# Kernel tuning notes

Measured on AMD Instinct MI355X. Metric: run time of the kernel, lower is better.

The kernel has to match this reference:

```python
import math
import jax, jax.numpy as jnp
import numpy as np

EPS = 1e-5

def _ln(x, g, b, axes):
    # LayerNormalization4D / 4DCF: mean/var (unbiased=False) over `axes`
    mu = x.mean(axis=axes, keepdims=True)
    var = ((x - mu) ** 2).mean(axis=axes, keepdims=True)
    return (x - mu) / jnp.sqrt(var + EPS) * g + b

def _prelu(x, a):
    return jnp.where(x >= 0, x, a * x)

def _unfold(x, ks, hs):
    # x: [N, C, Q] -> [N, L, C*ks]; patch layout (c, k) matches F.unfold
    N, C, Qd = x.shape
    L = (Qd - ks) // hs + 1
    idx = jnp.arange(L) * hs
    p = x[:, :, idx[:, None] + jnp.arange(ks)]  # [N, C, L, ks]
    return p.transpose(0, 2, 1, 3).reshape(N, L, C * ks)

def _lstm_dir(xs, Wi, Wh, bi, bh, H):
    # xs: [N, L, Cin]; torch gate order i, f, g, o
    xg = jnp.einsum('nlc,gc->nlg', xs, Wi) + bi + bh  # [N, L, 4H]
    def step(carry, gt):
        h, c = carry
        g = gt + h @ Wh.T
        i, f, gg, o = jnp.split(g, 4, axis=-1)
        c = jax.nn.sigmoid(f) * c + jax.nn.sigmoid(i) * jnp.tanh(gg)
        h = jax.nn.sigmoid(o) * jnp.tanh(c)
        return (h, c), h
    N = xs.shape[0]
    z = jnp.zeros((N, H), xs.dtype)
    _, hs = jax.lax.scan(step, (z, z), jnp.swapaxes(xg, 0, 1))
    return jnp.swapaxes(hs, 0, 1)

def _bilstm(x, wih, whh, bih, bhh):
    H = whh.shape[-1]
    f = _lstm_dir(x, wih[0], whh[0], bih[0], bhh[0], H)
    bk = _lstm_dir(x[:, ::-1], wih[1], whh[1], bih[1], bhh[1], H)[:, ::-1]
    return jnp.concatenate([f, bk], axis=-1)

def _convT1d(x, w, b):
    # x: [N, I, L]; w: [I, O, K] (torch ConvTranspose1d layout); stride 1
    K = w.shape[2]
    w2 = jnp.transpose(w, (1, 0, 2))[:, :, ::-1]
    y = jax.lax.conv_general_dilated(x, w2, (1,), [(K - 1, K - 1)],
                                     dimension_numbers=('NCH', 'OIH', 'NCH'))
    return y + b[None, :, None]

def _forward(x, mouth, intra_g, intra_b, intra_wih, intra_whh, intra_bih, intra_bhh,
             intra_lw, intra_lb, inter_g, inter_b, inter_wih, inter_whh, inter_bih,
             inter_bhh, inter_lw, inter_lb, qw, qb, qa, qg, qbe, kw, kb, ka, kg, kbe,
             vw, vb, va, vg, vbe, pw, pb, pa, pg, pbe):
    emb_ks, emb_hs = 4, 1
    B, C, oT, oQ = x.shape
    T = math.ceil((oT - emb_ks) / emb_hs) * emb_hs + emb_ks
    Qd = math.ceil((oQ - emb_ks) / emb_hs) * emb_hs + emb_ks
    x = jnp.pad(x, ((0, 0), (0, 0), (0, T - oT), (0, Qd - oQ)))
    inp = x
    # ---- intra (biLSTM along freq axis) ----
    h = _ln(inp, intra_g[None, :, None, None], intra_b[None, :, None, None], (1,))
    h = h.transpose(0, 2, 1, 3).reshape(B * T, C, Qd)
    h = _unfold(h, emb_ks, emb_hs)                          # [B*T, L, C*ks]
    h = _bilstm(h, intra_wih, intra_whh, intra_bih, intra_bhh)
    h = _convT1d(h.transpose(0, 2, 1), intra_lw, intra_lb)  # [B*T, C, Qd]
    intra = h.reshape(B, T, C, Qd).transpose(0, 2, 1, 3) + inp
    # ---- inter (biLSTM along time axis) ----
    h = _ln(intra, inter_g[None, :, None, None], inter_b[None, :, None, None], (1,))
    h = h.transpose(0, 3, 1, 2).reshape(B * Qd, C, T)
    h = _unfold(h, emb_ks, emb_hs)
    h = _bilstm(h, inter_wih, inter_whh, inter_bih, inter_bhh)
    h = _convT1d(h.transpose(0, 2, 1), inter_lw, inter_lb)  # [B*Qd, C, T]
    inter = h.reshape(B, Qd, C, T).transpose(0, 2, 3, 1) + intra
    inter = inter[..., :oT, :oQ]                             # [B, C, oT, oQ]
    # ---- multi-head full self-attention over time (conv1x1 QKV per head) ----
    NH = qw.shape[0]
    def qkv(w, b_, a_, g_, be_):
        y = jnp.einsum('bctf,hec->hbetf', inter, w) + b_[:, None, :, None, None]
        y = _prelu(y, a_[:, None, None, None, None])
        return _ln(y, g_[:, None, :, None, :], be_[:, None, :, None, :], (2, 4))
    Qh = qkv(qw, qb, qa, qg, qbe)   # [H, B, E, T, F]
    Kh = qkv(kw, kb, ka, kg, kbe)
    Vh = qkv(vw, vb, va, vg, vbe)   # [H, B, D, T, F]
    E = Qh.shape[2]; D = Vh.shape[2]; F = oQ
    q2 = Qh.transpose(0, 1, 3, 2, 4).reshape(NH, B, oT, E * F)
    k2 = Kh.transpose(0, 1, 3, 2, 4).reshape(NH, B, oT, E * F)
    v2 = Vh.transpose(0, 1, 3, 2, 4).reshape(NH, B, oT, D * F)
    scale = 1.0 / jnp.sqrt(jnp.asarray(E * F, x.dtype))
    attn = jax.nn.softmax(jnp.einsum('hbte,hbse->hbts', q2, k2) * scale, axis=-1)
    o = jnp.einsum('hbts,hbsd->hbtd', attn, v2).reshape(NH, B, oT, D, F)
    o = o.transpose(1, 0, 3, 2, 4).reshape(B, NH * D, oT, F)
    # ---- concat projection ----
    p = jnp.einsum('bctf,oc->botf', o, pw) + pb[None, :, None, None]
    p = _prelu(p, pa)
    p = _ln(p, pg[None, :, None, :], pbe[None, :, None, :], (1, 3))
    return p + inter

def setup_inputs() -> dict:
    key = jax.random.key(0)
    keys = iter(jax.random.split(key, 48))
    f32 = jnp.float32
    def nrm(shape, s=0.05):
        return jax.random.normal(next(keys), shape, f32) * s
    B, C, T, F = 2, 48, 512, 65
    K, H, NH, E = 4, 192, 4, 8
    Cin = C * K
    D = C // NH
    return {
        'x': jax.random.normal(next(keys), (B, C, T, F), f32),
        'mouth': jax.random.normal(next(keys), (B, 64), f32),
        'intra_g': jnp.ones((C,), f32), 'intra_b': jnp.zeros((C,), f32),
        'intra_wih': nrm((2, 4 * H, Cin)), 'intra_whh': nrm((2, 4 * H, H)),
        'intra_bih': nrm((2, 4 * H)), 'intra_bhh': nrm((2, 4 * H)),
        'intra_lw': nrm((2 * H, C, K)), 'intra_lb': nrm((C,)),
        'inter_g': jnp.ones((C,), f32), 'inter_b': jnp.zeros((C,), f32),
        'inter_wih': nrm((2, 4 * H, Cin)), 'inter_whh': nrm((2, 4 * H, H)),
        'inter_bih': nrm((2, 4 * H)), 'inter_bhh': nrm((2, 4 * H)),
        'inter_lw': nrm((2 * H, C, K)), 'inter_lb': nrm((C,)),
        'qw': nrm((NH, E, C)), 'qb': nrm((NH, E)), 'qa': 0.25 * jnp.ones((NH,), f32),
        'qg': jnp.ones((NH, E, F), f32), 'qbe': jnp.zeros((NH, E, F), f32),
        'kw': nrm((NH, E, C)), 'kb': nrm((NH, E)), 'ka': 0.25 * jnp.ones((NH,), f32),
        'kg': jnp.ones((NH, E, F), f32), 'kbe': jnp.zeros((NH, E, F), f32),
        'vw': nrm((NH, D, C)), 'vb': nrm((NH, D)), 'va': 0.25 * jnp.ones((NH,), f32),
        'vg': jnp.ones((NH, D, F), f32), 'vbe': jnp.zeros((NH, D, F), f32),
        'pw': nrm((C, C)), 'pb': nrm((C,)), 'pa': jnp.float32(0.25),
        'pg': jnp.ones((C, F), f32), 'pbe': jnp.zeros((C, F), f32),
    }

def reference(x, mouth, intra_g, intra_b, intra_wih, intra_whh, intra_bih, intra_bhh,
              intra_lw, intra_lb, inter_g, inter_b, inter_wih, inter_whh, inter_bih,
              inter_bhh, inter_lw, inter_lb, qw, qb, qa, qg, qbe, kw, kb, ka, kg, kbe,
              vw, vb, va, vg, vbe, pw, pb, pa, pg, pbe):
    return _forward(x, mouth, intra_g, intra_b, intra_wih, intra_whh, intra_bih,
                    intra_bhh, intra_lw, intra_lb, inter_g, inter_b, inter_wih,
                    inter_whh, inter_bih, inter_bhh, inter_lw, inter_lb, qw, qb, qa,
                    qg, qbe, kw, kb, ka, kg, kbe, vw, vb, va, vg, vbe, pw, pb, pa,
                    pg, pbe)
```

## Files before the change

### kernel.cpp

```cpp
#include <hip/hip_runtime.h>
#include <hip/hip_bf16.h>

typedef __bf16 bf16x8 __attribute__((ext_vector_type(8)));
typedef unsigned short u16x8 __attribute__((ext_vector_type(8)));
typedef float f32x4 __attribute__((ext_vector_type(4)));

#define DEV static __device__ __forceinline__

DEV unsigned short f2bf(float f){
  __hip_bfloat16 h = __float2bfloat16(f);
  return __builtin_bit_cast(unsigned short, h);
}
DEV float b2f(unsigned short u){
  return __bfloat162float(__builtin_bit_cast(__hip_bfloat16, u));
}
DEV float sig2(float xs){
  return __builtin_amdgcn_rcpf(1.0f + __builtin_amdgcn_exp2f(-xs));
}
DEV float tanh2s(float xs){
  return 1.0f - 2.0f*__builtin_amdgcn_rcpf(__builtin_amdgcn_exp2f(xs + xs) + 1.0f);
}
DEV float tanh_n(float x){
  return 1.0f - 2.0f*__builtin_amdgcn_rcpf(__builtin_amdgcn_exp2f(x * 2.885390082f) + 1.0f);
}
DEV void lds_barrier(){
  asm volatile("s_waitcnt lgkmcnt(0)\ns_barrier" ::: "memory");
}


__global__ void zero16(uint4* p, size_t n){
  size_t i = (size_t)blockIdx.x*blockDim.x + threadIdx.x;
  size_t st = (size_t)gridDim.x*blockDim.x;
  uint4 z = make_uint4(0u,0u,0u,0u);
  for (; i < n; i += st) p[i] = z;
}

__global__ void cast_bf(const float* __restrict__ s, unsigned short* __restrict__ d, int n, float scale){
  int i = blockIdx.x*256 + threadIdx.x;
  if (i < n) d[i] = f2bf(s[i]*scale);
}

__global__ void cast_wi(const float* __restrict__ s, unsigned short* __restrict__ d, float scale){
  int i = blockIdx.x*256 + threadIdx.x;
  if (i < 294912){
    int dn = i/192, k = i - dn*192;
    int c = k >> 2, kk = k & 3;
    d[(size_t)dn*192 + kk*48 + c] = f2bf(s[i]*scale);
  }
}

__global__ void bias_comb(const float* __restrict__ a, const float* __restrict__ b,
                          float* __restrict__ d, int n, float scale){
  int i = blockIdx.x*256 + threadIdx.x;
  if (i < n) d[i] = (a[i] + b[i])*scale;
}

__global__ void lwt_build(const float* __restrict__ lw, unsigned short* __restrict__ lwt){
  int i = blockIdx.x*256 + threadIdx.x;
  if (i < 384*48*4){
    int m = i / 192; int rest = i - m*192; int c = rest >> 2; int k = rest & 3;
    lwt[(size_t)c*1536 + k*384 + m] = f2bf(lw[i]);
  }
}

__global__ __launch_bounds__(256) void ln_unf_intra(
    const float* __restrict__ in, const float* __restrict__ g,
    const float* __restrict__ be, unsigned short* __restrict__ unf)
{
  int bt = blockIdx.x; int b = bt >> 9, t = bt & 511;
  __shared__ float v[48][66];
  __shared__ float mu[65], rs[65];
  __shared__ float g_l[48], b_l[48];
  const float* base = in + (size_t)b*(48*512*65) + (size_t)t*65;
  for (int i = threadIdx.x; i < 48*65; i += 256){
    int c = i/65, q = i - c*65;
    v[c][q] = base[(size_t)c*(512*65) + q];
  }
  if (threadIdx.x < 48){ g_l[threadIdx.x] = g[threadIdx.x]; b_l[threadIdx.x] = be[threadIdx.x]; }
  __syncthreads();
  if (threadIdx.x < 65){
    int q = threadIdx.x; float s=0.f, s2=0.f;
    #pragma unroll
    for (int c = 0; c < 48; c++){ float x = v[c][q]; s += x; s2 += x*x; }
    float m = s*(1.0f/48.0f);
    mu[q] = m; rs[q] = rsqrtf(s2*(1.0f/48.0f) - m*m + 1e-5f);
  }
  __syncthreads();
  unsigned short* orow = unf + (size_t)(b*512 + t)*62*192;
  for (int idx = threadIdx.x; idx < 62*24; idx += 256){
    int l = idx/24, jg = idx - l*24;
    int kk = jg/6, c0 = (jg - kk*6)*8;
    int q = l + kk;
    ushort4 p0, p1;
    float mq = mu[q], rq = rs[q];
    p0.x = f2bf((v[c0+0][q]-mq)*rq*g_l[c0+0] + b_l[c0+0]);
    p0.y = f2bf((v[c0+1][q]-mq)*rq*g_l[c0+1] + b_l[c0+1]);
    p0.z = f2bf((v[c0+2][q]-mq)*rq*g_l[c0+2] + b_l[c0+2]);
    p0.w = f2bf((v[c0+3][q]-mq)*rq*g_l[c0+3] + b_l[c0+3]);
    p1.x = f2bf((v[c0+4][q]-mq)*rq*g_l[c0+4] + b_l[c0+4]);
    p1.y = f2bf((v[c0+5][q]-mq)*rq*g_l[c0+5] + b_l[c0+5]);
    p1.z = f2bf((v[c0+6][q]-mq)*rq*g_l[c0+6] + b_l[c0+6]);
    p1.w = f2bf((v[c0+7][q]-mq)*rq*g_l[c0+7] + b_l[c0+7]);
    *(ushort4*)(orow + (size_t)l*192 + kk*48 + c0) = p0;
    *(ushort4*)(orow + (size_t)l*192 + kk*48 + c0 + 4) = p1;
  }
}

__global__ __launch_bounds__(256) void ln_unf_inter(
    const float* __restrict__ in, const float* __restrict__ g,
    const float* __restrict__ be, unsigned short* __restrict__ unf)
{
  int bt = blockIdx.x; int b = bt >> 9, t = bt & 511;
  __shared__ float v[48][66];
  __shared__ float mu[65], rs[65];
  __shared__ float g_l[48], b_l[48];
  const float* base = in + (size_t)b*(48*512*65) + (size_t)t*65;
  for (int i = threadIdx.x; i < 48*65; i += 256){
    int c = i/65, q = i - c*65;
    v[c][q] = base[(size_t)c*(512*65) + q];
  }
  if (threadIdx.x < 48){ g_l[threadIdx.x] = g[threadIdx.x]; b_l[threadIdx.x] = be[threadIdx.x]; }
  __syncthreads();
  if (threadIdx.x < 65){
    int q = threadIdx.x; float s=0.f, s2=0.f;
    #pragma unroll
    for (int c = 0; c < 48; c++){ float x = v[c][q]; s += x; s2 += x*x; }
    float m = s*(1.0f/48.0f);
    mu[q] = m; rs[q] = rsqrtf(s2*(1.0f/48.0f) - m*m + 1e-5f);
  }
  __syncthreads();
  for (int idx = threadIdx.x; idx < 4*65*6; idx += 256){
    int s = idx/390;
    int rem = idx - s*390;
    int q = rem/6, c0 = (rem - q*6)*8;
    int l = t - 3 + s, kk = 3 - s;
    if (l < 0 || l > 508) continue;
    float mq = mu[q], rq = rs[q];
    ushort4 p0, p1;
    p0.x = f2bf((v[c0+0][q]-mq)*rq*g_l[c0+0] + b_l[c0+0]);
    p0.y = f2bf((v[c0+1][q]-mq)*rq*g_l[c0+1] + b_l[c0+1]);
    p0.z = f2bf((v[c0+2][q]-mq)*rq*g_l[c0+2] + b_l[c0+2]);
    p0.w = f2bf((v[c0+3][q]-mq)*rq*g_l[c0+3] + b_l[c0+3]);
    p1.x = f2bf((v[c0+4][q]-mq)*rq*g_l[c0+4] + b_l[c0+4]);
    p1.y = f2bf((v[c0+5][q]-mq)*rq*g_l[c0+5] + b_l[c0+5]);
    p1.z = f2bf((v[c0+6][q]-mq)*rq*g_l[c0+6] + b_l[c0+6]);
    p1.w = f2bf((v[c0+7][q]-mq)*rq*g_l[c0+7] + b_l[c0+7]);
    size_t addr = ((size_t)(b*65+q)*509 + l)*192 + kk*48 + c0;
    *(ushort4*)(unf + addr) = p0;
    *(ushort4*)(unf + addr + 4) = p1;
  }
}

__global__ __launch_bounds__(256) void gemm_xg(
    const unsigned short* __restrict__ unf, const unsigned short* __restrict__ wib,
    const float* __restrict__ bias, unsigned short* __restrict__ xg,
    int NSEQ, int TW, int win0, int L, int nvalid)
{
  const int d = blockIdx.z;
  const int lane = threadIdx.x & 63, wave = threadIdx.x >> 6;
  const int kg = lane >> 4, lr = lane & 15;
  const int nslb = TW >> 3;
  const int sb  = blockIdx.x / nslb;
  const int slb = blockIdx.x - sb*nslb;
  const int nbase = blockIdx.y*64;
  const unsigned short* Bp = wib + (size_t)d*768*192;

  const unsigned short* abase[2];
  #pragma unroll
  for (int mt = 0; mt < 2; mt++){
    int sl = slb*8 + wave*2 + mt;
    int s = win0 + sl;
    int l = d ? (L-1-s) : s;
    l = l < 0 ? 0 : (l > L-1 ? L-1 : l);
    int seq = sb*16 + lr;
    seq = seq < nvalid ? seq : nvalid-1;
    abase[mt] = unf + ((size_t)seq*L + l)*192;
  }

  f32x4 acc[2][4] = {};
  #pragma unroll
  for (int kt = 0; kt < 6; kt++){
    int k0 = kt*32 + kg*8;
    bf16x8 a0 = *(const bf16x8*)(abase[0] + k0);
    bf16x8 a1 = *(const bf16x8*)(abase[1] + k0);
    #pragma unroll
    for (int nt = 0; nt < 4; nt++){
      int n = nbase + nt*16 + lr;
      bf16x8 bfr = *(const bf16x8*)(Bp + (size_t)n*192 + k0);
      acc[0][nt] = __builtin_amdgcn_mfma_f32_16x16x32_bf16(a0, bfr, acc[0][nt], 0,0,0);
      acc[1][nt] = __builtin_amdgcn_mfma_f32_16x16x32_bf16(a1, bfr, acc[1][nt], 0,0,0);
    }
  }
  #pragma unroll
  for (int mt = 0; mt < 2; mt++){
    int sl = slb*8 + wave*2 + mt;
    size_t rowb = (((size_t)d*(NSEQ>>4) + sb)*TW + sl)*768;
    #pragma unroll
    for (int nt = 0; nt < 4; nt++){
      int n = nbase + nt*16 + lr;
      float bs = bias[d*768 + n];
      ushort4 pk;
      pk.x = f2bf(acc[mt][nt][0] + bs);
      pk.y = f2bf(acc[mt][nt][1] + bs);
      pk.z = f2bf(acc[mt][nt][2] + bs);
      pk.w = f2bf(acc[mt][nt][3] + bs);
      *(ushort4*)(xg + (rowb + n)*16 + kg*4) = pk;
    }
  }
}

__global__ __launch_bounds__(768, 3) void lstm_rec(
    const unsigned short* __restrict__ xg,
    const unsigned short* __restrict__ whb,
    unsigned short* __restrict__ hs,
    float* __restrict__ state,
    int NSEQ, int TW, int win0, int L, int Qrows, int nvalid, int steps)
{
  const int d = blockIdx.y;
  const int seq0 = blockIdx.x * 16;
  const int tid = threadIdx.x;
  const int lane = tid & 63, w = tid >> 6;
  const int kg = lane >> 4, lr = lane & 15;
  const int col = w*16 + lr;

  __shared__ unsigned short h_lds[2][16][200];

  bf16x8 whf[4][6];
  #pragma unroll
  for (int g = 0; g < 4; g++){
    const unsigned short* wrow = whb + ((size_t)d*768 + g*192 + col)*192;
    #pragma unroll
    for (int kt = 0; kt < 6; kt++)
      whf[g][kt] = *(const bf16x8*)(wrow + kt*32 + kg*8);
  }

  float c_reg[4];
  unsigned short* hsp[4];
  bool val[4];
  const int l0 = d ? (L-1-win0) : win0;
  const ptrdiff_t ldelta = d ? -384 : 384;
  #pragma unroll
  for (int r = 0; r < 4; r++){
    int m = kg*4 + r;
    const float* st = state + (((size_t)d*NSEQ + seq0 + m)*2)*192;
    h_lds[0][m][col] = f2bf(st[col]);
    c_reg[r] = st[192 + col];
    val[r] = (seq0 + m) < nvalid;
    hsp[r] = hs + ((size_t)(seq0+m)*Qrows + (l0+3))*384 + d*192 + col;
  }
  lds_barrier();

  const unsigned short* xq0 = xg + ((((size_t)d*(NSEQ>>4) + blockIdx.x)*TW)*768)*16
                              + ((size_t)col)*16 + kg*4;
  const size_t SSTR = (size_t)768*16;

  uint2 pfA[4], pfB[4];
  {
    const unsigned short* p1 = xq0 + (steps > 1 ? SSTR : 0);
    #pragma unroll
    for (int g = 0; g < 4; g++){
      pfA[g] = *(const uint2*)(xq0 + (size_t)g*(192*16));
      pfB[g] = *(const uint2*)(p1  + (size_t)g*(192*16));
    }
  }

  int cur = 0;
  auto do_step = [&](uint2 (&pf)[4], int ss){
    f32x4 acc[4];
    #pragma unroll
    for (int g = 0; g < 4; g++){
      unsigned int lo = pf[g].x, hi = pf[g].y;
      acc[g][0] = b2f((unsigned short)(lo & 0xffffu));
      acc[g][1] = b2f((unsigned short)(lo >> 16));
      acc[g][2] = b2f((unsigned short)(hi & 0xffffu));
      acc[g][3] = b2f((unsigned short)(hi >> 16));
    }
    int nss = ss + 2; nss = nss > steps-1 ? steps-1 : nss;
    const unsigned short* np = xq0 + (size_t)nss*SSTR;
    #pragma unroll
    for (int g = 0; g < 4; g++)
      pf[g] = *(const uint2*)(np + (size_t)g*(192*16));
    #pragma unroll
    for (int kt = 0; kt < 6; kt++){
      bf16x8 a = *(const bf16x8*)(&h_lds[cur][lr][kt*32 + kg*8]);
      #pragma unroll
      for (int g = 0; g < 4; g++)
        acc[g] = __builtin_amdgcn_mfma_f32_16x16x32_bf16(a, whf[g][kt], acc[g], 0,0,0);
    }
    #pragma unroll
    for (int r = 0; r < 4; r++){
      float gi = sig2(acc[0][r]);
      float gf = sig2(acc[1][r]);
      float gg = tanh2s(acc[2][r]);
      float go = sig2(acc[3][r]);
      float c = gf*c_reg[r] + gi*gg;
      c_reg[r] = c;
      float h = go*tanh_n(c);
      unsigned short hb = f2bf(h);
      h_lds[cur^1][kg*4 + r][col] = hb;
      if (val[r]) *hsp[r] = hb;
      hsp[r] += ldelta;
    }
    lds_barrier();
    cur ^= 1;
  };

  for (int ss = 0; ss < steps; ss += 2){
    do_step(pfA, ss);
    if (ss + 1 < steps) do_step(pfB, ss + 1);
  }

  #pragma unroll
  for (int r = 0; r < 4; r++){
    int m = kg*4 + r;
    float* st = state + (((size_t)d*NSEQ + seq0 + m)*2)*192;
    st[col] = b2f(h_lds[cur][m][col]);
    st[192 + col] = c_reg[r];
  }
}

template<int MODE>
__global__ __launch_bounds__(256) void gemm_convt(
    const unsigned short* __restrict__ hs, const unsigned short* __restrict__ lwt,
    const float* __restrict__ lb, const float* __restrict__ addsrc, float* __restrict__ dst)
{
  constexpr int Q  = MODE ? 512 : 65;
  const int lane = threadIdx.x & 63, wave = threadIdx.x >> 6;
  const int kg = lane >> 4, lr = lane & 15;
  const int R0 = blockIdx.x * 64;

  __shared__ union U {
    unsigned short a[70][392];
    float c[64][52];
  } sm;

  const int HB0 = R0 + 3*(R0/Q);
  for (int idx = threadIdx.x; idx < 70*48; idx += 256){
    int j = idx/48, seg = idx - j*48;
    *(uint4*)&sm.a[j][seg*8] = *(const uint4*)(hs + ((size_t)(HB0+j))*384 + seg*8);
  }
  __syncthreads();

  const int row = R0 + wave*16 + lr;
  const int an = row / Q;
  const int jb = row + 3*an - HB0;

  f32x4 acc[4] = {};
  for (int kt = 0; kt < 48; kt++){
    int k0 = kt*32 + kg*8;
    int tap = k0 / 384;
    int m0 = k0 - tap*384;
    bf16x8 a = *(const bf16x8*)(&sm.a[jb + 3 - tap][m0]);
    #pragma unroll
    for (int nt = 0; nt < 4; nt++){
      bf16x8 bfr = *(const bf16x8*)(lwt + (size_t)(nt*16+lr)*1536 + k0);
      acc[nt] = __builtin_amdgcn_mfma_f32_16x16x32_bf16(a, bfr, acc[nt], 0,0,0);
    }
  }

  if (MODE == 0){
    __syncthreads();
    #pragma unroll
    for (int nt = 0; nt < 3; nt++)
      #pragma unroll
      for (int r = 0; r < 4; r++)
        sm.c[wave*16 + kg*4 + r][nt*16 + lr] = acc[nt][r];
    __syncthreads();
    const int b = R0 >= 33280 ? 1 : 0;
    const size_t bb = (size_t)b*1597440;
    const int rb = R0 - b*33280;
    for (int idx = threadIdx.x; idx < 48*16; idx += 256){
      int n = idx >> 4, g = idx & 15;
      size_t off = bb + (size_t)n*33280 + rb + g*4;
      float4 av = *(const float4*)(addsrc + off);
      float lbn = lb[n];
      float4 o;
      o.x = sm.c[g*4+0][n] + lbn + av.x;
      o.y = sm.c[g*4+1][n] + lbn + av.y;
      o.z = sm.c[g*4+2][n] + lbn + av.z;
      o.w = sm.c[g*4+3][n] + lbn + av.w;
      *(float4*)(dst + off) = o;
    }
  } else {
    #pragma unroll
    for (int nt = 0; nt < 3; nt++){
      int n = nt*16 + lr;
      float lbn = lb[n];
      #pragma unroll
      for (int r = 0; r < 4; r++){
        int orow = R0 + wave*16 + kg*4 + r;
        int ns = orow >> 9, t = orow & 511;
        size_t off = (size_t)(ns/65)*1597440 + (size_t)n*33280 + (ns%65) + (size_t)t*65;
        dst[off] = acc[nt][r] + lbn + addsrc[off];
      }
    }
  }
}

__global__ __launch_bounds__(256) void gemm_rm(
    const unsigned short* __restrict__ A, const unsigned short* __restrict__ B, float* __restrict__ C,
    int lda, int ldb, int ldc, int KT, int nmax, long long strA, long long strB, long long strC)
{
  const int z = blockIdx.z;
  A += (size_t)z * strA; B += (size_t)z * strB; C += (size_t)z * strC;
  const int lane = threadIdx.x & 63, wave = threadIdx.x >> 6;
  const int kg = lane >> 4, lr = lane & 15;
  const int rowbase = blockIdx.x*128 + wave*32;
  const int nbase = blockIdx.y*64;
  f32x4 acc[2][4] = {};
  for (int kt = 0; kt < KT; kt++){
    int k0 = kt*32 + kg*8;
    bf16x8 a0 = *(const bf16x8*)(A + (size_t)(rowbase+lr)*lda + k0);
    bf16x8 a1 = *(const bf16x8*)(A + (size_t)(rowbase+16+lr)*lda + k0);
    #pragma unroll
    for (int nt = 0; nt < 4; nt++){
      bf16x8 bfr = *(const bf16x8*)(B + (size_t)(nbase+nt*16+lr)*ldb + k0);
      acc[0][nt] = __builtin_amdgcn_mfma_f32_16x16x32_bf16(a0, bfr, acc[0][nt], 0,0,0);
      acc[1][nt] = __builtin_amdgcn_mfma_f32_16x16x32_bf16(a1, bfr, acc[1][nt], 0,0,0);
    }
  }
  #pragma unroll
  for (int mt = 0; mt < 2; mt++)
  #pragma unroll
  for (int nt = 0; nt < 4; nt++)
  #pragma unroll
  for (int r = 0; r < 4; r++){
    int n = nbase + nt*16 + lr;
    if (n < nmax){
      int row = rowbase + mt*16 + kg*4 + r;
      C[(size_t)row*ldc + n] = acc[mt][nt][r];
    }
  }
}

__global__ __launch_bounds__(256) void qkv_k(
    const float* __restrict__ inter, const float* __restrict__ w, const float* __restrict__ bias,
    const float* __restrict__ alpha, const float* __restrict__ gam, const float* __restrict__ bet,
    unsigned short* __restrict__ out, int E, int mode)
{
  int t = blockIdx.x; int hb = blockIdx.y; int h = hb >> 1, b = hb & 1;
  __shared__ float in_l[48][66];
  __shared__ float w_l[12][48];
  __shared__ float y_l[780];
  __shared__ float rs1[4], rs2[4];
  const float* base = inter + (size_t)b*(48*512*65) + (size_t)t*65;
  for (int i = threadIdx.x; i < 48*65; i += 256){
    int c = i/65, f = i - c*65;
    in_l[c][f] = base[(size_t)c*(512*65) + f];
  }
  for (int i = threadIdx.x; i < E*48; i += 256) w_l[i/48][i - (i/48)*48] = w[(size_t)h*E*48 + i];
  __syncthreads();
  int nel = E*65;
  float a = alpha[h];
  float ps = 0.f, pq = 0.f;
  for (int i = threadIdx.x; i < nel; i += 256){
    int e = i/65, f = i - e*65;
    float s = bias[h*E + e];
    #pragma unroll
    for (int c = 0; c < 48; c++) s += w_l[e][c]*in_l[c][f];
    s = s >= 0.f ? s : a*s;
    y_l[i] = s; ps += s; pq += s*s;
  }
  #pragma unroll
  for (int o = 32; o; o >>= 1){ ps += __shfl_xor(ps, o); pq += __shfl_xor(pq, o); }
  if ((threadIdx.x & 63) == 0){ rs1[threadIdx.x>>6] = ps; rs2[threadIdx.x>>6] = pq; }
  __syncthreads();
  ps = rs1[0]+rs1[1]+rs1[2]+rs1[3]; pq = rs2[0]+rs2[1]+rs2[2]+rs2[3];
  float inv = 1.0f/(float)nel;
  float m = ps*inv; float rstd = rsqrtf(pq*inv - m*m + 1e-5f);
  for (int i = threadIdx.x; i < nel; i += 256){
    int e = i/65, f = i - e*65;
    float v = (y_l[i]-m)*rstd*gam[(size_t)(h*E+e)*65 + f] + bet[(size_t)(h*E+e)*65 + f];
    if (mode < 2) out[((size_t)hb*512 + t)*544 + i] = f2bf(v);
    else          out[((size_t)hb*832 + i)*512 + t] = f2bf(v);
  }
}

__global__ __launch_bounds__(256) void softmax_k(const float* __restrict__ S, unsigned short* __restrict__ P){
  size_t row = (size_t)blockIdx.y*512 + blockIdx.x;
  const float* s = S + row*512;
  int tid = threadIdx.x;
  float v0 = s[tid], v1 = s[tid+256];
  float m = fmaxf(v0, v1);
  #pragma unroll
  for (int o = 32; o; o >>= 1) m = fmaxf(m, __shfl_xor(m, o));
  __shared__ float r4[4], q4[4];
  if ((tid & 63) == 0) r4[tid>>6] = m;
  __syncthreads();
  m = fmaxf(fmaxf(r4[0], r4[1]), fmaxf(r4[2], r4[3]));
  const float sc = 0.04385290096535146f;
  float e0 = __expf((v0-m)*sc), e1 = __expf((v1-m)*sc);
  float su = e0 + e1;
  #pragma unroll
  for (int o = 32; o; o >>= 1) su += __shfl_xor(su, o);
  if ((tid & 63) == 0) q4[tid>>6] = su;
  __syncthreads();
  su = q4[0]+q4[1]+q4[2]+q4[3];
  float inv = __builtin_amdgcn_rcpf(su);
  unsigned short* p = P + row*512;
  p[tid] = f2bf(e0*inv); p[tid+256] = f2bf(e1*inv);
}

__global__ __launch_bounds__(256) void pout_k(
    const float* __restrict__ o, const float* __restrict__ pw, const float* __restrict__ pb,
    const float* __restrict__ pa, const float* __restrict__ pg, const float* __restrict__ pbe,
    const float* __restrict__ inter, float* __restrict__ out)
{
  int bt = blockIdx.x; int b = bt >> 9, t = bt & 511;
  __shared__ float o_l[48][66];
  __shared__ float pw_l[48][48];
  __shared__ float p_l[3120];
  __shared__ float rs1[4], rs2[4];
  for (int i = threadIdx.x; i < 48*65; i += 256){
    int c = i/65, f = i - c*65; int h = c/12, dd = c - h*12;
    o_l[c][f] = o[((size_t)(h*2+b)*512 + t)*780 + dd*65 + f];
  }
  for (int i = threadIdx.x; i < 48*48; i += 256) pw_l[i/48][i - (i/48)*48] = pw[i];
  __syncthreads();
  float a = pa[0];
  float ps = 0.f, pq = 0.f;
  for (int i = threadIdx.x; i < 3120; i += 256){
    int oc = i/65, f = i - oc*65;
    float s = pb[oc];
    #pragma unroll
    for (int c = 0; c < 48; c++) s += pw_l[oc][c]*o_l[c][f];
    s = s >= 0.f ? s : a*s;
    p_l[i] = s; ps += s; pq += s*s;
  }
  #pragma unroll
  for (int o2 = 32; o2; o2 >>= 1){ ps += __shfl_xor(ps, o2); pq += __shfl_xor(pq, o2); }
  if ((threadIdx.x & 63) == 0){ rs1[threadIdx.x>>6] = ps; rs2[threadIdx.x>>6] = pq; }
  __syncthreads();
  ps = rs1[0]+rs1[1]+rs1[2]+rs1[3]; pq = rs2[0]+rs2[1]+rs2[2]+rs2[3];
  float m = ps*(1.0f/3120.0f); float rstd = rsqrtf(pq*(1.0f/3120.0f) - m*m + 1e-5f);
  for (int i = threadIdx.x; i < 3120; i += 256){
    int oc = i/65, f = i - oc*65;
    size_t off = ((size_t)(b*48+oc)*512 + t)*65 + f;
    out[off] = (p_l[i]-m)*rstd*pg[i] + pbe[i] + inter[off];
  }
}


extern "C" void kernel_launch(void* const* d_in, const int* in_sizes, int n_in,
                              void* d_out, int out_size, void* d_ws, size_t ws_size,
                              hipStream_t stream)
{
  const float* x         = (const float*)d_in[0];
  const float* intra_g   = (const float*)d_in[2];
  const float* intra_b   = (const float*)d_in[3];
  const float* intra_wih = (const float*)d_in[4];
  const float* intra_whh = (const float*)d_in[5];
  const float* intra_bih = (const float*)d_in[6];
  const float* intra_bhh = (const float*)d_in[7];
  const float* intra_lw  = (const float*)d_in[8];
  const float* intra_lb  = (const float*)d_in[9];
  const float* inter_g   = (const float*)d_in[10];
  const float* inter_b   = (const float*)d_in[11];
  const float* inter_wih = (const float*)d_in[12];
  const float* inter_whh = (const float*)d_in[13];
  const float* inter_bih = (const float*)d_in[14];
  const float* inter_bhh = (const float*)d_in[15];
  const float* inter_lw  = (const float*)d_in[16];
  const float* inter_lb  = (const float*)d_in[17];
  const float* qw  = (const float*)d_in[18];
  const float* qb  = (const float*)d_in[19];
  const float* qa  = (const float*)d_in[20];
  const float* qg  = (const float*)d_in[21];
  const float* qbe = (const float*)d_in[22];
  const float* kw  = (const float*)d_in[23];
  const float* kb  = (const float*)d_in[24];
  const float* ka  = (const float*)d_in[25];
  const float* kgm = (const float*)d_in[26];
  const float* kbe = (const float*)d_in[27];
  const float* vw  = (const float*)d_in[28];
  const float* vb  = (const float*)d_in[29];
  const float* va  = (const float*)d_in[30];
  const float* vg  = (const float*)d_in[31];
  const float* vbe = (const float*)d_in[32];
  const float* pw  = (const float*)d_in[33];
  const float* pb  = (const float*)d_in[34];
  const float* pa  = (const float*)d_in[35];
  const float* pgm = (const float*)d_in[36];
  const float* pbe = (const float*)d_in[37];

  char* ws = (char*)d_ws;
  constexpr size_t WIB_INTRA = 0;
  constexpr size_t WHB_INTRA = 589824;
  constexpr size_t WIB_INTER = 1179648;
  constexpr size_t WHB_INTER = 1769472;
  constexpr size_t LWT_INTRA = 2359296;
  constexpr size_t LWT_INTER = 2555904;
  constexpr size_t BIAS_INTRA = 2752512;
  constexpr size_t BIAS_INTER = 2758656;
  constexpr size_t UNF   = 2764800;
  constexpr size_t INTER = 2764800;
  constexpr size_t STATE = 28311552;
  constexpr size_t HS    = 31457280;
  constexpr size_t INTRA = 84934656;
  constexpr size_t XG    = 97714176;
  constexpr size_t Q2B   = XG;
  constexpr size_t K2B   = XG + 4456448;
  constexpr size_t V2T   = XG + 8912896;
  constexpr size_t SCORES= XG + 15728640;
  constexpr size_t ATTNB = XG + 24117248;
  constexpr size_t OBUF  = XG + 28311552;

  auto U16 = [&](size_t off){ return (unsigned short*)(ws + off); };
  auto F32 = [&](size_t off){ return (float*)(ws + off); };

  const float LOG2E = 1.4426950408889634f;

  zero16<<<512,256,0,stream>>>((uint4*)(ws+LWT_INTRA), 393216/16);
  cast_wi<<<1152,256,0,stream>>>(intra_wih, U16(WIB_INTRA), LOG2E);
  cast_bf<<<1152,256,0,stream>>>(intra_whh, U16(WHB_INTRA), 294912, LOG2E);
  cast_wi<<<1152,256,0,stream>>>(inter_wih, U16(WIB_INTER), LOG2E);
  cast_bf<<<1152,256,0,stream>>>(inter_whh, U16(WHB_INTER), 294912, LOG2E);
  bias_comb<<<6,256,0,stream>>>(intra_bih, intra_bhh, F32(BIAS_INTRA), 1536, LOG2E);
  bias_comb<<<6,256,0,stream>>>(inter_bih, inter_bhh, F32(BIAS_INTER), 1536, LOG2E);
  lwt_build<<<288,256,0,stream>>>(intra_lw, U16(LWT_INTRA));
  lwt_build<<<288,256,0,stream>>>(inter_lw, U16(LWT_INTER));

  ln_unf_intra<<<1024,256,0,stream>>>(x, intra_g, intra_b, U16(UNF));
  zero16<<<2048,256,0,stream>>>((uint4*)(ws+HS), 53477376/16);
  zero16<<<2048,256,0,stream>>>((uint4*)(ws+STATE), 3145728/16);
  for (int w = 0; w < 4; w++){
    int win0 = w*16;
    int steps = (62 - win0) < 16 ? (62 - win0) : 16;
    gemm_xg<<<dim3(128,12,2),256,0,stream>>>(U16(UNF), U16(WIB_INTRA), F32(BIAS_INTRA), U16(XG),
                                             1024, 16, win0, 62, 1024);
    lstm_rec<<<dim3(64,2),768,0,stream>>>(U16(XG), U16(WHB_INTRA), U16(HS), F32(STATE),
                                          1024, 16, win0, 62, 68, 1024, steps);
  }
  gemm_convt<0><<<1040,256,0,stream>>>(U16(HS), U16(LWT_INTRA), intra_lb, x, F32(INTRA));

  ln_unf_inter<<<1024,256,0,stream>>>(F32(INTRA), inter_g, inter_b, U16(UNF));
  zero16<<<2048,256,0,stream>>>((uint4*)(ws+HS), 51417600/16);
  zero16<<<2048,256,0,stream>>>((uint4*)(ws+STATE), 3145728/16);
  for (int w = 0; w < 8; w++){
    int win0 = w*64;
    int steps = (509 - win0) < 64 ? (509 - win0) : 64;
    gemm_xg<<<dim3(72,12,2),256,0,stream>>>(U16(UNF), U16(WIB_INTER), F32(BIAS_INTER), U16(XG),
                                            144, 64, win0, 509, 130);
    lstm_rec<<<dim3(9,2),768,0,stream>>>(U16(XG), U16(WHB_INTER), U16(HS), F32(STATE),
                                         144, 64, win0, 509, 515, 130, steps);
  }
  gemm_convt<1><<<1040,256,0,stream>>>(U16(HS), U16(LWT_INTER), inter_lb, F32(INTRA), F32(INTER));

  zero16<<<2048,256,0,stream>>>((uint4*)(ws+Q2B), 15728640/16);
  qkv_k<<<dim3(512,8),256,0,stream>>>(F32(INTER), qw, qb, qa, qg, qbe, U16(Q2B), 8, 0);
  qkv_k<<<dim3(512,8),256,0,stream>>>(F32(INTER), kw, kb, ka, kgm, kbe, U16(K2B), 8, 1);
  qkv_k<<<dim3(512,8),256,0,stream>>>(F32(INTER), vw, vb, va, vg, vbe, U16(V2T), 12, 2);
  gemm_rm<<<dim3(4,8,8),256,0,stream>>>(U16(Q2B), U16(K2B), F32(SCORES),
                                        544, 544, 512, 17, 512,
                                        (long long)512*544, (long long)512*544, (long long)512*512);
  softmax_k<<<dim3(512,8),256,0,stream>>>(F32(SCORES), U16(ATTNB));
  gemm_rm<<<dim3(4,13,8),256,0,stream>>>(U16(ATTNB), U16(V2T), F32(OBUF),
                                         512, 512, 780, 16, 780,
                                         (long long)512*512, (long long)832*512, (long long)512*780);
  pout_k<<<1024,256,0,stream>>>(F32(OBUF), pw, pb, pa, pgm, pbe, F32(INTER), (float*)d_out);
}
```

Measured before the change: 1.960 ms.

## Overlap next-window input GEMM with LSTM recurrence via fused double-buffered kernel

Merges the input-projection GEMM for the next time window into the recurrent LSTM launch. Extra blocks compute the next window's gate inputs into a second buffer while the recurrent blocks consume the current one, so the GEMM no longer sits serially between recurrence steps. Window sizes are halved (8 and 32 steps), which doubles the number of launches. The full zeroing of the hidden-state buffer is replaced by zeroing only its pad rows, and the LDS tile in the conv-transpose GEMM is re-laid out to avoid bank conflicts. The risk is that the extra GEMM blocks compete with the latency-bound recurrence blocks for compute units and slow them down.

```diff
diff --git a/kernel.cpp b/kernel.cpp
--- a/kernel.cpp
+++ b/kernel.cpp
@@ -33,6 +33,17 @@
   size_t st = (size_t)gridDim.x*blockDim.x;
   uint4 z = make_uint4(0u,0u,0u,0u);
   for (; i < n; i += st) p[i] = z;
+}
+
+__global__ void zero_pads(unsigned short* hs, int NSEQ, int Qrows, int L){
+  int i = blockIdx.x*256 + threadIdx.x;
+  int total = NSEQ*6*384;
+  if (i < total){
+    int t = i/(6*384); int rem = i - t*(6*384);
+    int r = rem/384, c = rem - r*384;
+    int row = r < 3 ? r : L + r;
+    hs[((size_t)t*Qrows + row)*384 + c] = 0;
+  }
 }
 
 __global__ void cast_bf(const float* __restrict__ s, unsigned short* __restrict__ d, int n, float scale){
@@ -209,21 +220,69 @@
   }
 }
 
-__global__ __launch_bounds__(768, 3) void lstm_rec(
-    const unsigned short* __restrict__ xg,
+__global__ __launch_bounds__(768, 3) void fused_rec_xg(
+    const unsigned short* __restrict__ xgA,
     const unsigned short* __restrict__ whb,
     unsigned short* __restrict__ hs,
     float* __restrict__ state,
-    int NSEQ, int TW, int win0, int L, int Qrows, int nvalid, int steps)
-{
-  const int d = blockIdx.y;
-  const int seq0 = blockIdx.x * 16;
+    const unsigned short* __restrict__ unf,
+    const unsigned short* __restrict__ wib,
+    const float* __restrict__ bias,
+    unsigned short* __restrict__ xgB,
+    int NSEQ, int TW, int win0, int L, int Qrows, int nvalid, int steps,
+    int NR, int NSBR, int NSLB, int win0x)
+{
   const int tid = threadIdx.x;
   const int lane = tid & 63, w = tid >> 6;
   const int kg = lane >> 4, lr = lane & 15;
+
+  __shared__ unsigned short h_lds[2][16][200];
+
+  if ((int)blockIdx.x >= NR){
+    int e = blockIdx.x - NR;
+    int nb = e % 12; e /= 12;
+    int slb = e % NSLB; e /= NSLB;
+    int sb = e % NSBR; int d = e / NSBR;
+    int sl = slb*12 + w;
+    if (sl >= TW) return;
+    int s = win0x + sl;
+    int l = d ? (L-1-s) : s;
+    l = l < 0 ? 0 : (l > L-1 ? L-1 : l);
+    int seq = sb*16 + lr;
+    seq = seq < nvalid ? seq : nvalid-1;
+    const unsigned short* ab = unf + ((size_t)seq*L + l)*192;
+    const unsigned short* Bp = wib + (size_t)d*768*192;
+    const int nbase = nb*64;
+    f32x4 acc[4] = {};
+    #pragma unroll
+    for (int kt = 0; kt < 6; kt++){
+      int k0 = kt*32 + kg*8;
+      bf16x8 a = *(const bf16x8*)(ab + k0);
+      #pragma unroll
+      for (int nt = 0; nt < 4; nt++){
+        bf16x8 bfr = *(const bf16x8*)(Bp + (size_t)(nbase+nt*16+lr)*192 + k0);
+        acc[nt] = __builtin_amdgcn_mfma_f32_16x16x32_bf16(a, bfr, acc[nt], 0,0,0);
+      }
+    }
+    size_t rowb = (((size_t)d*NSBR + sb)*TW + sl)*768;
+    #pragma unroll
+    for (int nt = 0; nt < 4; nt++){
+      int n = nbase + nt*16 + lr;
+      float bs = bias[d*768 + n];
+      ushort4 pk;
+      pk.x = f2bf(acc[nt][0] + bs);
+      pk.y = f2bf(acc[nt][1] + bs);
+      pk.z = f2bf(acc[nt][2] + bs);
+      pk.w = f2bf(acc[nt][3] + bs);
+      *(ushort4*)(xgB + (rowb + n)*16 + kg*4) = pk;
+    }
+    return;
+  }
+
+  const int d = blockIdx.x / NSBR;
+  const int sbx = blockIdx.x - d*NSBR;
+  const int seq0 = sbx * 16;
   const int col = w*16 + lr;
-
-  __shared__ unsigned short h_lds[2][16][200];
 
   bf16x8 whf[4][6];
   #pragma unroll
@@ -250,7 +309,7 @@
   }
   lds_barrier();
 
-  const unsigned short* xq0 = xg + ((((size_t)d*(NSEQ>>4) + blockIdx.x)*TW)*768)*16
+  const unsigned short* xq0 = xgA + ((((size_t)d*NSBR + sbx)*TW)*768)*16
                               + ((size_t)col)*16 + kg*4;
   const size_t SSTR = (size_t)768*16;
 
@@ -330,14 +389,14 @@
   const int R0 = blockIdx.x * 64;
 
   __shared__ union U {
-    unsigned short a[70][392];
+    unsigned short a[27328];
     float c[64][52];
   } sm;
 
   const int HB0 = R0 + 3*(R0/Q);
   for (int idx = threadIdx.x; idx < 70*48; idx += 256){
     int j = idx/48, seg = idx - j*48;
-    *(uint4*)&sm.a[j][seg*8] = *(const uint4*)(hs + ((size_t)(HB0+j))*384 + seg*8);
+    *(uint4*)&sm.a[(seg*71 + j)*8] = *(const uint4*)(hs + ((size_t)(HB0+j))*384 + seg*8);
   }
   __syncthreads();
 
@@ -349,8 +408,8 @@
   for (int kt = 0; kt < 48; kt++){
     int k0 = kt*32 + kg*8;
     int tap = k0 / 384;
-    int m0 = k0 - tap*384;
-    bf16x8 a = *(const bf16x8*)(&sm.a[jb + 3 - tap][m0]);
+    int slot = (k0 >> 3) - tap*48;
+    bf16x8 a = *(const bf16x8*)&sm.a[(slot*71 + jb + 3 - tap)*8];
     #pragma unroll
     for (int nt = 0; nt < 4; nt++){
       bf16x8 bfr = *(const bf16x8*)(lwt + (size_t)(nt*16+lr)*1536 + k0);
@@ -620,31 +679,45 @@
   lwt_build<<<288,256,0,stream>>>(intra_lw, U16(LWT_INTRA));
   lwt_build<<<288,256,0,stream>>>(inter_lw, U16(LWT_INTER));
 
-  ln_unf_intra<<<1024,256,0,stream>>>(x, intra_g, intra_b, U16(UNF));
-  zero16<<<2048,256,0,stream>>>((uint4*)(ws+HS), 53477376/16);
-  zero16<<<2048,256,0,stream>>>((uint4*)(ws+STATE), 3145728/16);
-  for (int w = 0; w < 4; w++){
-    int win0 = w*16;
-    int steps = (62 - win0) < 16 ? (62 - win0) : 16;
-    gemm_xg<<<dim3(128,12,2),256,0,stream>>>(U16(UNF), U16(WIB_INTRA), F32(BIAS_INTRA), U16(XG),
-                                             1024, 16, win0, 62, 1024);
-    lstm_rec<<<dim3(64,2),768,0,stream>>>(U16(XG), U16(WHB_INTRA), U16(HS), F32(STATE),
-                                          1024, 16, win0, 62, 68, 1024, steps);
-  }
-  gemm_convt<0><<<1040,256,0,stream>>>(U16(HS), U16(LWT_INTRA), intra_lb, x, F32(INTRA));
-
-  ln_unf_inter<<<1024,256,0,stream>>>(F32(INTRA), inter_g, inter_b, U16(UNF));
-  zero16<<<2048,256,0,stream>>>((uint4*)(ws+HS), 51417600/16);
-  zero16<<<2048,256,0,stream>>>((uint4*)(ws+STATE), 3145728/16);
-  for (int w = 0; w < 8; w++){
-    int win0 = w*64;
-    int steps = (509 - win0) < 64 ? (509 - win0) : 64;
-    gemm_xg<<<dim3(72,12,2),256,0,stream>>>(U16(UNF), U16(WIB_INTER), F32(BIAS_INTER), U16(XG),
-                                            144, 64, win0, 509, 130);
-    lstm_rec<<<dim3(9,2),768,0,stream>>>(U16(XG), U16(WHB_INTER), U16(HS), F32(STATE),
-                                         144, 64, win0, 509, 515, 130, steps);
-  }
-  gemm_convt<1><<<1040,256,0,stream>>>(U16(HS), U16(LWT_INTER), inter_lb, F32(INTRA), F32(INTER));
+  {
+    unsigned short* xb[2] = { U16(XG), U16(XG + 25165824) };
+    ln_unf_intra<<<1024,256,0,stream>>>(x, intra_g, intra_b, U16(UNF));
+    zero_pads<<<9216,256,0,stream>>>(U16(HS), 1024, 68, 62);
+    zero16<<<2048,256,0,stream>>>((uint4*)(ws+STATE), 3145728/16);
+    gemm_xg<<<dim3(64,12,2),256,0,stream>>>(U16(UNF), U16(WIB_INTRA), F32(BIAS_INTRA), xb[0],
+                                            1024, 8, 0, 62, 1024);
+    for (int w = 0; w < 8; w++){
+      int win0 = w*8;
+      int steps = (62 - win0) < 8 ? (62 - win0) : 8;
+      int nxg = (w < 7) ? 1536 : 0;
+      fused_rec_xg<<<128 + nxg, 768, 0, stream>>>(
+          xb[w&1], U16(WHB_INTRA), U16(HS), F32(STATE),
+          U16(UNF), U16(WIB_INTRA), F32(BIAS_INTRA), xb[(w+1)&1],
+          1024, 8, win0, 62, 68, 1024, steps,
+          128, 64, 1, (w+1)*8);
+    }
+    gemm_convt<0><<<1040,256,0,stream>>>(U16(HS), U16(LWT_INTRA), intra_lb, x, F32(INTRA));
+  }
+
+  {
+    unsigned short* xb[2] = { U16(XG), U16(XG + 14155776) };
+    ln_unf_inter<<<1024,256,0,stream>>>(F32(INTRA), inter_g, inter_b, U16(UNF));
+    zero_pads<<<1170,256,0,stream>>>(U16(HS), 130, 515, 509);
+    zero16<<<2048,256,0,stream>>>((uint4*)(ws+STATE), 3145728/16);
+    gemm_xg<<<dim3(36,12,2),256,0,stream>>>(U16(UNF), U16(WIB_INTER), F32(BIAS_INTER), xb[0],
+                                            144, 32, 0, 509, 130);
+    for (int w = 0; w < 16; w++){
+      int win0 = w*32;
+      int steps = (509 - win0) < 32 ? (509 - win0) : 32;
+      int nxg = (w < 15) ? 648 : 0;
+      fused_rec_xg<<<18 + nxg, 768, 0, stream>>>(
+          xb[w&1], U16(WHB_INTER), U16(HS), F32(STATE),
+          U16(UNF), U16(WIB_INTER), F32(BIAS_INTER), xb[(w+1)&1],
+          144, 32, win0, 509, 515, 130, steps,
+          18, 9, 3, (w+1)*32);
+    }
+    gemm_convt<1><<<1040,256,0,stream>>>(U16(HS), U16(LWT_INTER), inter_lb, F32(INTRA), F32(INTER));
+  }
 
   zero16<<<2048,256,0,stream>>>((uint4*)(ws+Q2B), 15728640/16);
   qkv_k<<<dim3(512,8),256,0,stream>>>(F32(INTER), qw, qb, qa, qg, qbe, U16(Q2B), 8, 0);
```

Result: faster. 1.829 ms (-6.7%).
